# Kernel tuning notes

Hardware: AMD Instinct MI355X
Metric: run time of the kernel (lower is better)

## Reference

```python
import jax, jax.numpy as jnp
import numpy as np

# Haar (db1) analysis filters, matching the torch buffers exactly.
_SQRT2_INV = 0.7071067811865476
_H0 = jnp.array([_SQRT2_INV, _SQRT2_INV], dtype=jnp.float32)
_H1 = jnp.array([-_SQRT2_INV, _SQRT2_INV], dtype=jnp.float32)


def setup_inputs() -> dict:
    key = jax.random.key(0)
    x = jax.random.normal(key, (16, 3, 1024, 1024), dtype=jnp.float32)
    return {
        "x": x,
        "h0_h": _H0.reshape(1, 1, 1, 2),  # horizontal lowpass  (OIHW)
        "h1_h": _H1.reshape(1, 1, 1, 2),  # horizontal highpass
        "h0_v": _H0.reshape(1, 1, 2, 1),  # vertical lowpass
        "h1_v": _H1.reshape(1, 1, 2, 1),  # vertical highpass
    }


def _conv(x, k, stride):
    # torch F.conv2d == cross-correlation; lax conv is also cross-correlation (no flip).
    return jax.lax.conv_general_dilated(
        x, k, window_strides=stride, padding="VALID",
        dimension_numbers=("NCHW", "OIHW", "NCHW"))


def _dwt(x, h0_h, h1_h, h0_v, h1_v):
    B, C, H, W = x.shape
    taps = h0_h.shape[-1]
    pad = taps - 1
    # zero-pad on the left (width), then horizontal filtering with stride 2 in W
    xp = jnp.pad(x, ((0, 0), (0, 0), (0, 0), (pad, 0))).reshape(B * C, 1, H, W + pad)
    x_h0 = _conv(xp, h0_h, (1, 2))  # (B*C,1,H,W_out)
    x_h1 = _conv(xp, h1_h, (1, 2))
    # zero-pad on the top (height), then vertical filtering with stride 2 in H
    x_h0 = jnp.pad(x_h0, ((0, 0), (0, 0), (pad, 0), (0, 0)))
    x_h1 = jnp.pad(x_h1, ((0, 0), (0, 0), (pad, 0), (0, 0)))
    LL = _conv(x_h0, h0_v, (2, 1))
    LH = _conv(x_h0, h1_v, (2, 1))
    HL = _conv(x_h1, h0_v, (2, 1))
    HH = _conv(x_h1, h1_v, (2, 1))
    Hf, Wf = LL.shape[-2], LL.shape[-1]
    rs = lambda t: t.reshape(B, C, Hf, Wf)
    return rs(LL), (rs(LH), rs(HL), rs(HH))


def reference(x, h0_h, h1_h, h0_v, h1_v):
    return _dwt(x, h0_h, h1_h, h0_v, h1_v)
```

## Files before the change

kernel.cpp:

```cpp
#include <hip/hip_runtime.h>


typedef float fx4 __attribute__((ext_vector_type(4)));
typedef float fx2 __attribute__((ext_vector_type(2)));

__device__ __forceinline__ void haar_row(float hT, fx4 vT, float hB, fx4 vB,
                                         fx2& ll, fx2& lh, fx2& hl, fx2& hh)
{
    float a0 = hT,   b0 = vT.x, c0 = hB,   d0 = vB.x;
    float a1 = vT.y, b1 = vT.z, c1 = vB.y, d1 = vB.z;

    float st0 = a0 + b0, dt0 = b0 - a0, sb0 = c0 + d0, db0 = d0 - c0;
    float st1 = a1 + b1, dt1 = b1 - a1, sb1 = c1 + d1, db1 = d1 - c1;

    ll = fx2{0.5f * (st0 + sb0), 0.5f * (st1 + sb1)};
    lh = fx2{0.5f * (sb0 - st0), 0.5f * (sb1 - st1)};
    hl = fx2{0.5f * (dt0 + db0), 0.5f * (dt1 + db1)};
    hh = fx2{0.5f * (db0 - dt0), 0.5f * (db1 - dt1)};
}

__global__ __launch_bounds__(256) void dwt_haar_kernel(
    const float* __restrict__ x, float* __restrict__ out, int n_bc)
{
    constexpr int W  = 1024;
    constexpr int Ho = 512;
    constexpr int Wo = 512;

    const long long S = (long long)n_bc * Ho * Wo;

    int g   = blockIdx.x * 256 + threadIdx.x;
    int jp  = g & 255;
    int rem = g >> 8;
    int i2  = rem & 255;
    int bc  = rem >> 8;

    const int c0 = jp << 2;
    const float* rB = x + ((long long)bc << 20) + (long long)(i2 << 2) * W + c0;

    fx4 vB = *(const fx4*)(rB);
    fx4 vC = *(const fx4*)(rB + W);
    fx4 vD = *(const fx4*)(rB + 2 * W);
    fx4 vA = fx4{0.f, 0.f, 0.f, 0.f};
    const bool have_top = (i2 > 0);
    if (have_top) vA = *(const fx4*)(rB - W);

    float hA = __shfl_up(vA.w, 1);
    float hB = __shfl_up(vB.w, 1);
    float hC = __shfl_up(vC.w, 1);
    float hD = __shfl_up(vD.w, 1);
    if ((threadIdx.x & 63) == 0) {
        if (jp == 0) {
            hA = hB = hC = hD = 0.f;
        } else {
            hB = rB[-1];
            hC = rB[W - 1];
            hD = rB[2 * W - 1];
            hA = have_top ? rB[-W - 1] : 0.f;
        }
    }

    fx2 ll0, lh0, hl0, hh0, ll1, lh1, hl1, hh1;
    haar_row(hA, vA, hB, vB, ll0, lh0, hl0, hh0);
    haar_row(hC, vC, hD, vD, ll1, lh1, hl1, hh1);

    const long long obase0 = ((long long)bc * Ho + 2 * i2) * Wo + (jp << 1);
    const long long obase1 = obase0 + Wo;

    __builtin_nontemporal_store(ll0, (fx2*)(out +         obase0));
    __builtin_nontemporal_store(lh0, (fx2*)(out +     S + obase0));
    __builtin_nontemporal_store(hl0, (fx2*)(out + 2 * S + obase0));
    __builtin_nontemporal_store(hh0, (fx2*)(out + 3 * S + obase0));
    __builtin_nontemporal_store(ll1, (fx2*)(out +         obase1));
    __builtin_nontemporal_store(lh1, (fx2*)(out +     S + obase1));
    __builtin_nontemporal_store(hl1, (fx2*)(out + 2 * S + obase1));
    __builtin_nontemporal_store(hh1, (fx2*)(out + 3 * S + obase1));
}

extern "C" void kernel_launch(void* const* d_in, const int* in_sizes, int n_in,
                              void* d_out, int out_size, void* d_ws, size_t ws_size,
                              hipStream_t stream) {
    const float* x = (const float*)d_in[0];
    float* out = (float*)d_out;

    const int n_bc = in_sizes[0] / (1024 * 1024);
    const long long total_threads = (long long)n_bc * 256 * 256;
    const int blocks = (int)(total_threads / 256);

    dwt_haar_kernel<<<blocks, 256, 0, stream>>>(x, out, n_bc);
}
```

Measured before the change: 348.6 us.

## Process multiple row-strips per block with double-buffered register prefetch

Each block now handles ITERS consecutive row-strips instead of one. The loads for the next strip are issued before the current strip is computed and stored, using two register buffers. The goal is to overlap global-load latency with compute and stores and to cut the block count and per-block launch overhead. In exchange, each thread holds more registers, and with fewer blocks the GPU may have less parallelism to hide memory latency.

New measurement: 351.4 us. No clear change (+0.8%).

```diff
diff --git a/kernel.cpp b/kernel.cpp
--- a/kernel.cpp
+++ b/kernel.cpp
@@ -4,67 +4,65 @@
 typedef float fx4 __attribute__((ext_vector_type(4)));
 typedef float fx2 __attribute__((ext_vector_type(2)));
 
+constexpr int ITERS = 6;
+
+struct Strip {
+    fx4 vA, vB, vC, vD;
+    float pA, pB, pC, pD;
+};
+
+__device__ __forceinline__ void issue(const float* __restrict__ x, int wi,
+                                      int c0, Strip& s)
+{
+    constexpr int W = 1024;
+    const int i2 = wi & 255, bc = wi >> 8;
+    const float* rB = x + ((long long)bc << 20) + (long long)(i2 << 2) * W + c0;
+    const bool have_top = (i2 != 0);
+
+    s.vB = *(const fx4*)(rB);
+    s.vC = *(const fx4*)(rB + W);
+    s.vD = *(const fx4*)(rB + 2 * W);
+    s.vA = fx4{0.f, 0.f, 0.f, 0.f};
+    if (have_top) s.vA = *(const fx4*)(rB - W);
+
+    s.pA = s.pB = s.pC = s.pD = 0.f;
+    if ((threadIdx.x & 63) == 0 && threadIdx.x != 0) {
+        s.pB = rB[-1];
+        s.pC = rB[W - 1];
+        s.pD = rB[2 * W - 1];
+        if (have_top) s.pA = rB[-W - 1];
+    }
+}
+
 __device__ __forceinline__ void haar_row(float hT, fx4 vT, float hB, fx4 vB,
                                          fx2& ll, fx2& lh, fx2& hl, fx2& hh)
 {
-    float a0 = hT,   b0 = vT.x, c0 = hB,   d0 = vB.x;
-    float a1 = vT.y, b1 = vT.z, c1 = vB.y, d1 = vB.z;
-
-    float st0 = a0 + b0, dt0 = b0 - a0, sb0 = c0 + d0, db0 = d0 - c0;
-    float st1 = a1 + b1, dt1 = b1 - a1, sb1 = c1 + d1, db1 = d1 - c1;
-
+    float st0 = hT + vT.x,   dt0 = vT.x - hT;
+    float sb0 = hB + vB.x,   db0 = vB.x - hB;
+    float st1 = vT.y + vT.z, dt1 = vT.z - vT.y;
+    float sb1 = vB.y + vB.z, db1 = vB.z - vB.y;
     ll = fx2{0.5f * (st0 + sb0), 0.5f * (st1 + sb1)};
     lh = fx2{0.5f * (sb0 - st0), 0.5f * (sb1 - st1)};
     hl = fx2{0.5f * (dt0 + db0), 0.5f * (dt1 + db1)};
     hh = fx2{0.5f * (db0 - dt0), 0.5f * (db1 - dt1)};
 }
 
-__global__ __launch_bounds__(256) void dwt_haar_kernel(
-    const float* __restrict__ x, float* __restrict__ out, int n_bc)
+__device__ __forceinline__ void process(float* __restrict__ out, long long S,
+                                        int wi, int jp, const Strip& s)
 {
-    constexpr int W  = 1024;
-    constexpr int Ho = 512;
-    constexpr int Wo = 512;
-
-    const long long S = (long long)n_bc * Ho * Wo;
-
-    int g   = blockIdx.x * 256 + threadIdx.x;
-    int jp  = g & 255;
-    int rem = g >> 8;
-    int i2  = rem & 255;
-    int bc  = rem >> 8;
-
-    const int c0 = jp << 2;
-    const float* rB = x + ((long long)bc << 20) + (long long)(i2 << 2) * W + c0;
-
-    fx4 vB = *(const fx4*)(rB);
-    fx4 vC = *(const fx4*)(rB + W);
-    fx4 vD = *(const fx4*)(rB + 2 * W);
-    fx4 vA = fx4{0.f, 0.f, 0.f, 0.f};
-    const bool have_top = (i2 > 0);
-    if (have_top) vA = *(const fx4*)(rB - W);
-
-    float hA = __shfl_up(vA.w, 1);
-    float hB = __shfl_up(vB.w, 1);
-    float hC = __shfl_up(vC.w, 1);
-    float hD = __shfl_up(vD.w, 1);
-    if ((threadIdx.x & 63) == 0) {
-        if (jp == 0) {
-            hA = hB = hC = hD = 0.f;
-        } else {
-            hB = rB[-1];
-            hC = rB[W - 1];
-            hD = rB[2 * W - 1];
-            hA = have_top ? rB[-W - 1] : 0.f;
-        }
-    }
+    float hA = __shfl_up(s.vA.w, 1);
+    float hB = __shfl_up(s.vB.w, 1);
+    float hC = __shfl_up(s.vC.w, 1);
+    float hD = __shfl_up(s.vD.w, 1);
+    if ((threadIdx.x & 63) == 0) { hA = s.pA; hB = s.pB; hC = s.pC; hD = s.pD; }
 
     fx2 ll0, lh0, hl0, hh0, ll1, lh1, hl1, hh1;
-    haar_row(hA, vA, hB, vB, ll0, lh0, hl0, hh0);
-    haar_row(hC, vC, hD, vD, ll1, lh1, hl1, hh1);
+    haar_row(hA, s.vA, hB, s.vB, ll0, lh0, hl0, hh0);
+    haar_row(hC, s.vC, hD, s.vD, ll1, lh1, hl1, hh1);
 
-    const long long obase0 = ((long long)bc * Ho + 2 * i2) * Wo + (jp << 1);
-    const long long obase1 = obase0 + Wo;
+    const int i2 = wi & 255, bc = wi >> 8;
+    const long long obase0 = ((long long)bc * 512 + 2 * i2) * 512 + (jp << 1);
+    const long long obase1 = obase0 + 512;
 
     __builtin_nontemporal_store(ll0, (fx2*)(out +         obase0));
     __builtin_nontemporal_store(lh0, (fx2*)(out +     S + obase0));
@@ -76,6 +74,34 @@
     __builtin_nontemporal_store(hh1, (fx2*)(out + 3 * S + obase1));
 }
 
+__global__ __launch_bounds__(256) void dwt_haar_kernel(
+    const float* __restrict__ x, float* __restrict__ out, int n_bc)
+{
+    const long long S = (long long)n_bc * 512 * 512;
+    const int wtot = n_bc * 256;
+    const int jp = threadIdx.x;
+    const int c0 = jp << 2;
+    const int w0 = blockIdx.x * ITERS;
+
+    if (w0 >= wtot) return;
+
+    Strip r0, r1;
+    issue(x, w0, c0, r0);
+
+#pragma unroll
+    for (int it = 0; it < ITERS; ++it) {
+        const int wi = w0 + it;
+        if (wi >= wtot) break;
+        if ((it & 1) == 0) {
+            if (it + 1 < ITERS && wi + 1 < wtot) issue(x, wi + 1, c0, r1);
+            process(out, S, wi, jp, r0);
+        } else {
+            if (it + 1 < ITERS && wi + 1 < wtot) issue(x, wi + 1, c0, r0);
+            process(out, S, wi, jp, r1);
+        }
+    }
+}
+
 extern "C" void kernel_launch(void* const* d_in, const int* in_sizes, int n_in,
                               void* d_out, int out_size, void* d_ws, size_t ws_size,
                               hipStream_t stream) {
@@ -83,8 +109,8 @@
     float* out = (float*)d_out;
 
     const int n_bc = in_sizes[0] / (1024 * 1024);
-    const long long total_threads = (long long)n_bc * 256 * 256;
-    const int blocks = (int)(total_threads / 256);
+    const int wtot = n_bc * 256;
+    const int blocks = (wtot + ITERS - 1) / ITERS;
 
     dwt_haar_kernel<<<blocks, 256, 0, stream>>>(x, out, n_bc);
 }
```

## Stage Haar subband outputs in LDS and write full rows with 16-byte stores

Applied to the files above, without the earlier changes.

Each block now covers a full 1024-wide strip of 8 input rows (two passes of the original per-thread work) and writes its four subband results into shared memory. After a barrier, each wavefront copies one subband's four output rows to global memory using contiguous float4 stores instead of scattered 8-byte stores. The goal is wider, fully coalesced writes. The cost is 32 KB of LDS per block, an extra LDS round trip and a barrier, and the nontemporal hint on output stores is dropped.

Measured after the change: 339.0 us. -2.7%, faster.

```diff
diff --git a/kernel.cpp b/kernel.cpp
--- a/kernel.cpp
+++ b/kernel.cpp
@@ -7,12 +7,10 @@
 __device__ __forceinline__ void haar_row(float hT, fx4 vT, float hB, fx4 vB,
                                          fx2& ll, fx2& lh, fx2& hl, fx2& hh)
 {
-    float a0 = hT,   b0 = vT.x, c0 = hB,   d0 = vB.x;
-    float a1 = vT.y, b1 = vT.z, c1 = vB.y, d1 = vB.z;
-
-    float st0 = a0 + b0, dt0 = b0 - a0, sb0 = c0 + d0, db0 = d0 - c0;
-    float st1 = a1 + b1, dt1 = b1 - a1, sb1 = c1 + d1, db1 = d1 - c1;
-
+    float st0 = hT + vT.x,   dt0 = vT.x - hT;
+    float sb0 = hB + vB.x,   db0 = vB.x - hB;
+    float st1 = vT.y + vT.z, dt1 = vT.z - vT.y;
+    float sb1 = vB.y + vB.z, db1 = vB.z - vB.y;
     ll = fx2{0.5f * (st0 + sb0), 0.5f * (st1 + sb1)};
     lh = fx2{0.5f * (sb0 - st0), 0.5f * (sb1 - st1)};
     hl = fx2{0.5f * (dt0 + db0), 0.5f * (dt1 + db1)};
@@ -22,58 +20,73 @@
 __global__ __launch_bounds__(256) void dwt_haar_kernel(
     const float* __restrict__ x, float* __restrict__ out, int n_bc)
 {
-    constexpr int W  = 1024;
-    constexpr int Ho = 512;
-    constexpr int Wo = 512;
-
+    constexpr int W = 1024, Ho = 512, Wo = 512;
     const long long S = (long long)n_bc * Ho * Wo;
 
-    int g   = blockIdx.x * 256 + threadIdx.x;
-    int jp  = g & 255;
-    int rem = g >> 8;
-    int i2  = rem & 255;
-    int bc  = rem >> 8;
+    __shared__ float lds[4 * 4 * 512];
 
+    const int t  = threadIdx.x;
+    const int bc = blockIdx.x >> 7;
+    const int T  = blockIdx.x & 127;
+    const int jp = t;
     const int c0 = jp << 2;
-    const float* rB = x + ((long long)bc << 20) + (long long)(i2 << 2) * W + c0;
 
-    fx4 vB = *(const fx4*)(rB);
-    fx4 vC = *(const fx4*)(rB + W);
-    fx4 vD = *(const fx4*)(rB + 2 * W);
-    fx4 vA = fx4{0.f, 0.f, 0.f, 0.f};
-    const bool have_top = (i2 > 0);
-    if (have_top) vA = *(const fx4*)(rB - W);
+#pragma unroll
+    for (int k = 0; k < 2; ++k) {
+        const int i2 = 2 * T + k;
+        const float* rB = x + ((long long)bc << 20) + (long long)(i2 << 2) * W + c0;
+        const bool have_top = (i2 != 0);
 
-    float hA = __shfl_up(vA.w, 1);
-    float hB = __shfl_up(vB.w, 1);
-    float hC = __shfl_up(vC.w, 1);
-    float hD = __shfl_up(vD.w, 1);
-    if ((threadIdx.x & 63) == 0) {
-        if (jp == 0) {
-            hA = hB = hC = hD = 0.f;
-        } else {
-            hB = rB[-1];
-            hC = rB[W - 1];
-            hD = rB[2 * W - 1];
-            hA = have_top ? rB[-W - 1] : 0.f;
+        fx4 vB = *(const fx4*)(rB);
+        fx4 vC = *(const fx4*)(rB + W);
+        fx4 vD = *(const fx4*)(rB + 2 * W);
+        fx4 vA = fx4{0.f, 0.f, 0.f, 0.f};
+        if (have_top) vA = *(const fx4*)(rB - W);
+
+        float hA = __shfl_up(vA.w, 1);
+        float hB = __shfl_up(vB.w, 1);
+        float hC = __shfl_up(vC.w, 1);
+        float hD = __shfl_up(vD.w, 1);
+        if ((t & 63) == 0) {
+            if (jp == 0) {
+                hA = hB = hC = hD = 0.f;
+            } else {
+                hB = rB[-1];
+                hC = rB[W - 1];
+                hD = rB[2 * W - 1];
+                hA = have_top ? rB[-W - 1] : 0.f;
+            }
         }
+
+        fx2 ll0, lh0, hl0, hh0, ll1, lh1, hl1, hh1;
+        haar_row(hA, vA, hB, vB, ll0, lh0, hl0, hh0);
+        haar_row(hC, vC, hD, vD, ll1, lh1, hl1, hh1);
+
+        const int r0 = 2 * k, r1 = 2 * k + 1;
+        const int cc = jp << 1;
+        *(fx2*)&lds[(0 * 4 + r0) * 512 + cc] = ll0;
+        *(fx2*)&lds[(1 * 4 + r0) * 512 + cc] = lh0;
+        *(fx2*)&lds[(2 * 4 + r0) * 512 + cc] = hl0;
+        *(fx2*)&lds[(3 * 4 + r0) * 512 + cc] = hh0;
+        *(fx2*)&lds[(0 * 4 + r1) * 512 + cc] = ll1;
+        *(fx2*)&lds[(1 * 4 + r1) * 512 + cc] = lh1;
+        *(fx2*)&lds[(2 * 4 + r1) * 512 + cc] = hl1;
+        *(fx2*)&lds[(3 * 4 + r1) * 512 + cc] = hh1;
     }
 
-    fx2 ll0, lh0, hl0, hh0, ll1, lh1, hl1, hh1;
-    haar_row(hA, vA, hB, vB, ll0, lh0, hl0, hh0);
-    haar_row(hC, vC, hD, vD, ll1, lh1, hl1, hh1);
+    __syncthreads();
 
-    const long long obase0 = ((long long)bc * Ho + 2 * i2) * Wo + (jp << 1);
-    const long long obase1 = obase0 + Wo;
-
-    __builtin_nontemporal_store(ll0, (fx2*)(out +         obase0));
-    __builtin_nontemporal_store(lh0, (fx2*)(out +     S + obase0));
-    __builtin_nontemporal_store(hl0, (fx2*)(out + 2 * S + obase0));
-    __builtin_nontemporal_store(hh0, (fx2*)(out + 3 * S + obase0));
-    __builtin_nontemporal_store(ll1, (fx2*)(out +         obase1));
-    __builtin_nontemporal_store(lh1, (fx2*)(out +     S + obase1));
-    __builtin_nontemporal_store(hl1, (fx2*)(out + 2 * S + obase1));
-    __builtin_nontemporal_store(hh1, (fx2*)(out + 3 * S + obase1));
+    const int w = t >> 6, l = t & 63;
+    float* obase = out + (long long)w * S
+                 + ((long long)bc * Ho + 4 * T) * Wo;
+#pragma unroll
+    for (int lr = 0; lr < 4; ++lr) {
+        const float* src = &lds[(w * 4 + lr) * 512];
+        fx4 a = *(const fx4*)(src + 4 * l);
+        fx4 b = *(const fx4*)(src + 4 * l + 256);
+        *(fx4*)(obase + lr * Wo + 4 * l)       = a;
+        *(fx4*)(obase + lr * Wo + 4 * l + 256) = b;
+    }
 }
 
 extern "C" void kernel_launch(void* const* d_in, const int* in_sizes, int n_in,
@@ -83,8 +96,6 @@
     float* out = (float*)d_out;
 
     const int n_bc = in_sizes[0] / (1024 * 1024);
-    const long long total_threads = (long long)n_bc * 256 * 256;
-    const int blocks = (int)(total_threads / 256);
-
+    const int blocks = n_bc * 128;
     dwt_haar_kernel<<<blocks, 256, 0, stream>>>(x, out, n_bc);
 }
```
